# Kernel optimization log

Measured on AMD Instinct MI355X. Metric: run time of the kernel, lower is better.

The kernel has to match this reference:

```python
import jax, jax.numpy as jnp
import numpy as np

B, S, D, H, F = 4, 2048, 256, 8, 2  # batch, seq, input_size, heads, mlp factor
EPS = 1e-5


def _ln(x, g, b):
    m = jnp.mean(x, axis=-1, keepdims=True)
    v = jnp.var(x, axis=-1, keepdims=True)
    return (x - m) / jnp.sqrt(v + EPS) * g + b


def setup_inputs() -> dict:
    key = jax.random.key(0)
    ks = jax.random.split(key, 12)
    s = 1.0 / np.sqrt(D)
    return {
        "X":  jax.random.normal(ks[0], (B, S, D), jnp.float32),
        # Wide attention: each of H heads has full [D,D] Q/K/V projections (no bias)
        "Wq": jax.random.uniform(ks[1], (H, D, D), jnp.float32, -s, s),
        "Wk": jax.random.uniform(ks[2], (H, D, D), jnp.float32, -s, s),
        "Wv": jax.random.uniform(ks[3], (H, D, D), jnp.float32, -s, s),
        "Wz": jax.random.uniform(ks[4], (H * D, D), jnp.float32, -1.0 / np.sqrt(H * D), 1.0 / np.sqrt(H * D)),
        "bz": jnp.zeros((D,), jnp.float32),
        "W1": jax.random.uniform(ks[5], (D, F * D), jnp.float32, -s, s),
        "b1": jnp.zeros((F * D,), jnp.float32),
        "W2": jax.random.uniform(ks[6], (F * D, D), jnp.float32, -1.0 / np.sqrt(F * D), 1.0 / np.sqrt(F * D)),
        "b2": jnp.zeros((D,), jnp.float32),
        "g1": jnp.ones((D,), jnp.float32),
        "be1": jnp.zeros((D,), jnp.float32),
        "g2": jnp.ones((D,), jnp.float32),
        "be2": jnp.zeros((D,), jnp.float32),
    }


def reference(X, Wq, Wk, Wv, Wz, bz, W1, b1, W2, b2, g1, be1, g2, be2):
    scale = D ** (-0.25)  # applied to both q and k as in the source
    q = jnp.einsum('bsd,hde->hbse', X, Wq) * scale   # [H,B,S,D]
    k = jnp.einsum('btd,hde->hbte', X, Wk) * scale
    v = jnp.einsum('btd,hde->hbte', X, Wv)
    attn = jax.nn.softmax(jnp.einsum('hbse,hbte->hbst', q, k), axis=-1)  # [H,B,S,S]
    zh = jnp.einsum('hbst,hbte->hbse', attn, v)       # [H,B,S,D]
    # concat heads along feature dim (head order matters for Wz)
    zcat = jnp.transpose(zh, (1, 2, 0, 3)).reshape(B, S, H * D)
    z = zcat @ Wz + bz
    z = _ln(z + X, g1, be1)                            # dropout p=0 -> identity
    z_ff = jnp.maximum(z @ W1 + b1, 0.0) @ W2 + b2
    z = _ln(z_ff + z, g2, be2)
    attn_mean = jnp.mean(attn, axis=0)                 # [B,S,S]
    return z, attn_mean
```

## Files before the change

kernel.cpp:

```cpp
#include <hip/hip_runtime.h>
#include <cstdint>
#include <cstddef>

#define B_  4
#define S_  2048
#define D_  256
#define H_  8
#define FD_ 512
#define N_  (B_*S_)
#define HD_ (H_*D_)
#define EPS 1e-5f

typedef __attribute__((ext_vector_type(8))) short bf16x8;
typedef __attribute__((ext_vector_type(8))) unsigned short u16x8;
typedef __attribute__((ext_vector_type(4))) float f32x4;

__device__ __forceinline__ unsigned short f2bf(float f) {
  union { float f; unsigned u; } x; x.f = f;
  unsigned u = x.u;
  return (unsigned short)((u + 0x7FFFu + ((u >> 16) & 1u)) >> 16);
}
__device__ __forceinline__ float bf2f(unsigned short h) {
  union { unsigned u; float f; } x; x.u = ((unsigned)h) << 16; return x.f;
}

__device__ __forceinline__ void glds16(const void* gptr, void* ldsptr) {
  __builtin_amdgcn_global_load_lds(
      (__attribute__((address_space(1))) void*)gptr,
      (__attribute__((address_space(3))) void*)ldsptr,
      16, 0, 0);
}

__device__ __forceinline__ int sw32(int row, int u) {
  return (row*32 + ((u & 24) | ((u & 7) ^ (row & 7)))) * 8;
}
__device__ __forceinline__ int sw16(int row, int u) {
  return (row*16 + ((u & 8) | ((u & 7) ^ (row & 7)))) * 8;
}

__global__ __launch_bounds__(256) void cast_x_kernel(
    const float* __restrict__ X, unsigned short* __restrict__ Xb)
{
  const size_t i8 = ((size_t)blockIdx.x * 256 + threadIdx.x) * 8;
  float4 a = *(const float4*)&X[i8];
  float4 b = *(const float4*)&X[i8 + 4];
  u16x8 o;
  o[0]=f2bf(a.x); o[1]=f2bf(a.y); o[2]=f2bf(a.z); o[3]=f2bf(a.w);
  o[4]=f2bf(b.x); o[5]=f2bf(b.y); o[6]=f2bf(b.z); o[7]=f2bf(b.w);
  *(u16x8*)&Xb[i8] = o;
}

__global__ __launch_bounds__(256) void prep_w_kernel(
    const float* __restrict__ Wq, const float* __restrict__ Wk,
    const float* __restrict__ Wv, unsigned short* __restrict__ Wt)
{
  __shared__ float tile[64][65];
  const int tid = threadIdx.x;
  const int d0 = blockIdx.x * 64, e0 = blockIdx.y * 64;
  const int w = blockIdx.z;
  const float* src;
  float scale;
  if (w < 8)       { src = Wq + (size_t)w*D_*D_;      scale = 0.25f; }
  else if (w < 16) { src = Wk + (size_t)(w-8)*D_*D_;  scale = 0.25f; }
  else             { src = Wv + (size_t)(w-16)*D_*D_; scale = 1.0f;  }
  {
    int r = tid >> 2, c16 = (tid & 3) * 16;
    const float* s = src + (size_t)(d0 + r)*D_ + e0 + c16;
    #pragma unroll
    for (int u = 0; u < 4; ++u) *(float4*)&tile[r][c16 + u*4] = *(const float4*)(s + u*4);
  }
  __syncthreads();
  {
    int er = tid >> 2, dc = (tid & 3) * 16;
    u16x8 o0, o1;
    #pragma unroll
    for (int j = 0; j < 8; ++j) {
      o0[j] = f2bf(tile[dc + j][er] * scale);
      o1[j] = f2bf(tile[dc + 8 + j][er] * scale);
    }
    unsigned short* dst = Wt + ((size_t)w*D_ + e0 + er)*D_ + d0 + dc;
    *(u16x8*)(dst)     = o0;
    *(u16x8*)(dst + 8) = o1;
  }
}

__global__ __launch_bounds__(256) void tcast_kernel(
    const float* __restrict__ src, unsigned short* __restrict__ dst,
    int R, int C)
{
  __shared__ float tile[64][65];
  const int tid = threadIdx.x;
  const int r0 = blockIdx.x * 64, c0 = blockIdx.y * 64;
  {
    int r = tid >> 2, c16 = (tid & 3) * 16;
    const float* s = src + (size_t)(r0 + r)*C + c0 + c16;
    #pragma unroll
    for (int u = 0; u < 4; ++u) *(float4*)&tile[r][c16 + u*4] = *(const float4*)(s + u*4);
  }
  __syncthreads();
  {
    int cr = tid >> 2, rc = (tid & 3) * 16;
    u16x8 o0, o1;
    #pragma unroll
    for (int j = 0; j < 8; ++j) {
      o0[j] = f2bf(tile[rc + j][cr]);
      o1[j] = f2bf(tile[rc + 8 + j][cr]);
    }
    unsigned short* d = dst + (size_t)(c0 + cr)*R + r0 + rc;
    *(u16x8*)(d)     = o0;
    *(u16x8*)(d + 8) = o1;
  }
}

__global__ __launch_bounds__(256) void qkv_kernel(
    const unsigned short* __restrict__ Xb, const unsigned short* __restrict__ Wt,
    unsigned short* __restrict__ q, unsigned short* __restrict__ k,
    unsigned short* __restrict__ v)
{
  __shared__ unsigned short Xt[64*32*8];
  __shared__ unsigned short Wtile[64*32*8];
  const int tid = threadIdx.x;
  const int w4 = tid >> 6, lane = tid & 63;
  const int c = lane & 15, qd = lane >> 4;
  const int n0 = blockIdx.x * 64;
  const int e0 = blockIdx.y * 64;
  const int w  = blockIdx.z;

  unsigned short* obase;
  if (w < 8)       obase = q + (size_t)w*N_*D_;
  else if (w < 16) obase = k + (size_t)(w-8)*N_*D_;
  else             obase = v + (size_t)(w-16)*N_*D_;

  {
    const char* xg = (const char*)Xb + (size_t)n0*512;
    const char* wg = (const char*)Wt + ((size_t)w*D_ + e0)*512;
    #pragma unroll
    for (int i = 0; i < 8; ++i) {
      int g = w4*8 + i;
      int r = 2*g + (lane >> 5);
      int su = lane & 31;
      int u = (su & 24) | ((su & 7) ^ (r & 7));
      glds16(xg + (size_t)r*512 + u*16, &Xt[g*512]);
      glds16(wg + (size_t)r*512 + u*16, &Wtile[g*512]);
    }
  }
  __syncthreads();

  f32x4 sc[4];
  #pragma unroll
  for (int nc = 0; nc < 4; ++nc) sc[nc] = (f32x4){0.f,0.f,0.f,0.f};
  #pragma unroll
  for (int ks = 0; ks < 8; ++ks) {
    bf16x8 xa = *(const bf16x8*)&Xt[sw32(16*w4 + c, ks*4 + qd)];
    #pragma unroll
    for (int nc = 0; nc < 4; ++nc) {
      bf16x8 bf = *(const bf16x8*)&Wtile[sw32(nc*16 + c, ks*4 + qd)];
      sc[nc] = __builtin_amdgcn_mfma_f32_16x16x32_bf16(xa, bf, sc[nc], 0, 0, 0);
    }
  }
  #pragma unroll
  for (int nc = 0; nc < 4; ++nc)
    #pragma unroll
    for (int r = 0; r < 4; ++r)
      obase[(size_t)(n0 + 16*w4 + qd*4 + r)*D_ + e0 + nc*16 + c] = f2bf(sc[nc][r]);
}

__global__ __launch_bounds__(256) void vtrans_kernel(
    const unsigned short* __restrict__ vb, unsigned short* __restrict__ vT)
{
  __shared__ unsigned short tile[64][72];
  const int tid = threadIdx.x;
  const int t0 = blockIdx.x * 64, e0 = blockIdx.y * 64;
  const int h = blockIdx.z >> 2, b = blockIdx.z & 3;
  const size_t in_base = (size_t)h*N_*D_ + (size_t)b*S_*D_;
  {
    int r = tid >> 2, c16 = (tid & 3) * 16;
    const unsigned short* src = vb + in_base + (size_t)(t0 + r)*D_ + e0 + c16;
    *(u16x8*)&tile[r][c16]     = *(const u16x8*)(src);
    *(u16x8*)&tile[r][c16 + 8] = *(const u16x8*)(src + 8);
  }
  __syncthreads();
  {
    int er = tid >> 2, tt = (tid & 3) * 16;
    u16x8 o0, o1;
    #pragma unroll
    for (int j = 0; j < 8; ++j) { o0[j] = tile[tt+j][er]; o1[j] = tile[tt+8+j][er]; }
    unsigned short* dst = vT + ((size_t)(h*4 + b)*D_ + e0 + er)*S_ + t0 + tt;
    *(u16x8*)(dst)     = o0;
    *(u16x8*)(dst + 8) = o1;
  }
}

__global__ __launch_bounds__(256, 2) void attn_ol_kernel(
    const unsigned short* __restrict__ qb, const unsigned short* __restrict__ kb,
    const unsigned short* __restrict__ vT, unsigned short* __restrict__ zcatb,
    float* __restrict__ Lws)
{
  __shared__ unsigned short Kt[2][32*32*8];
  __shared__ unsigned short Vt[2][16*544];
  __shared__ unsigned short ps[4][32][40];
  const int tid = threadIdx.x;
  const int w = tid >> 6, lane = tid & 63;
  const int c = lane & 15, qd = lane >> 4;
  const int s0 = blockIdx.x * 128;
  const int b = blockIdx.y, h = blockIdx.z;

  const size_t qkbase = (size_t)h*N_*D_ + (size_t)b*S_*D_;

  bf16x8 qa[2][8];
  #pragma unroll
  for (int mi = 0; mi < 2; ++mi) {
    const unsigned short* qrow = qb + qkbase + (size_t)(s0 + 32*w + 16*mi + c)*D_ + qd*8;
    #pragma unroll
    for (int ks = 0; ks < 8; ++ks) qa[mi][ks] = *(const bf16x8*)(qrow + ks*32);
  }

  f32x4 o[2][16];
  #pragma unroll
  for (int mi = 0; mi < 2; ++mi)
    #pragma unroll
    for (int i = 0; i < 16; ++i) o[mi][i] = (f32x4){0.f,0.f,0.f,0.f};
  float Lp[2][4] = {};

  const char* kB = (const char*)(kb + qkbase);
  const char* vB = (const char*)(vT + (size_t)(h*4 + b)*D_*S_);

  #define STAGE_OL(kt_, bi_)                                                   \
    {                                                                          \
      _Pragma("unroll")                                                        \
      for (int i = 0; i < 4; ++i) {                                            \
        int g = w*4 + i;                                                       \
        int r = 2*g + (lane >> 5);                                             \
        int su = lane & 31;                                                    \
        int u = (su & 24) | ((su & 7) ^ (r & 7));                              \
        glds16(kB + ((size_t)(kt_)*32 + r)*512 + u*16, &Kt[bi_][g*512]);       \
      }                                                                        \
      _Pragma("unroll")                                                        \
      for (int i = 0; i < 4; ++i) {                                            \
        int g = w*4 + i;                                                       \
        int e = g*16 + (lane >> 2);                                            \
        int qv = (lane & 3) ^ ((lane >> 3) & 3);                               \
        glds16(vB + (size_t)e*4096 + (size_t)(kt_)*64 + qv*16, &Vt[bi_][g*544]);\
      }                                                                        \
    }

  STAGE_OL(0, 0);

  for (int kt = 0; kt < 64; ++kt) {
    const int bi = kt & 1;
    __syncthreads();
    if (kt + 1 < 64) STAGE_OL(kt + 1, bi ^ 1);

    f32x4 sc[2][2];
    #pragma unroll
    for (int mi = 0; mi < 2; ++mi)
      #pragma unroll
      for (int nc = 0; nc < 2; ++nc) sc[mi][nc] = (f32x4){0.f,0.f,0.f,0.f};
    #pragma unroll
    for (int ks = 0; ks < 8; ++ks) {
      bf16x8 kf0 = *(const bf16x8*)&Kt[bi][sw32(c,      ks*4 + qd)];
      bf16x8 kf1 = *(const bf16x8*)&Kt[bi][sw32(16 + c, ks*4 + qd)];
      #pragma unroll
      for (int mi = 0; mi < 2; ++mi) {
        sc[mi][0] = __builtin_amdgcn_mfma_f32_16x16x32_bf16(qa[mi][ks], kf0, sc[mi][0], 0, 0, 0);
        sc[mi][1] = __builtin_amdgcn_mfma_f32_16x16x32_bf16(qa[mi][ks], kf1, sc[mi][1], 0, 0, 0);
      }
    }
    #pragma unroll
    for (int mi = 0; mi < 2; ++mi)
      #pragma unroll
      for (int nc = 0; nc < 2; ++nc)
        #pragma unroll
        for (int r = 0; r < 4; ++r) {
          float p = __expf(sc[mi][nc][r]);
          Lp[mi][r] += p;
          ps[w][mi*16 + qd*4 + r][nc*16 + c] = f2bf(p);
        }
    bf16x8 pa0 = *(const bf16x8*)&ps[w][c][qd*8];
    bf16x8 pa1 = *(const bf16x8*)&ps[w][16 + c][qd*8];
    #pragma unroll
    for (int ec = 0; ec < 16; ++ec) {
      bf16x8 vf = *(const bf16x8*)&Vt[bi][ec*544 + c*32 + (qd ^ ((c >> 1) & 3))*8];
      o[0][ec] = __builtin_amdgcn_mfma_f32_16x16x32_bf16(pa0, vf, o[0][ec], 0, 0, 0);
      o[1][ec] = __builtin_amdgcn_mfma_f32_16x16x32_bf16(pa1, vf, o[1][ec], 0, 0, 0);
    }
  }

  #pragma unroll
  for (int mi = 0; mi < 2; ++mi) {
    float il[4];
    #pragma unroll
    for (int r = 0; r < 4; ++r) {
      float L = Lp[mi][r];
      L += __shfl_xor(L, 1); L += __shfl_xor(L, 2);
      L += __shfl_xor(L, 4); L += __shfl_xor(L, 8);
      Lp[mi][r] = L;
      il[r] = 1.0f / L;
    }
    if (c == 0) {
      #pragma unroll
      for (int r = 0; r < 4; ++r)
        Lws[(size_t)h*N_ + b*S_ + s0 + 32*w + 16*mi + qd*4 + r] = Lp[mi][r];
    }
    #pragma unroll
    for (int ec = 0; ec < 16; ++ec)
      #pragma unroll
      for (int r = 0; r < 4; ++r)
        zcatb[(size_t)(b*S_ + s0 + 32*w + 16*mi + qd*4 + r)*HD_ + h*D_ + ec*16 + c] =
            f2bf(o[mi][ec][r] * il[r]);
  }
  #undef STAGE_OL
}

__global__ __launch_bounds__(256, 2) void attn_mean_kernel(
    const unsigned short* __restrict__ qb, const unsigned short* __restrict__ kb,
    const float* __restrict__ Lws, float* __restrict__ out_attn)
{
  __shared__ unsigned short Kt[2][64*32*8];
  const int tid = threadIdx.x;
  const int w = tid >> 6, lane = tid & 63;
  const int c = lane & 15, qd = lane >> 4;
  const int s0 = blockIdx.x * 128;
  const int t0 = blockIdx.y * 64;
  const int b = blockIdx.z;

  float am[2][4][4] = {};

  #define STAGE_AM(h_, bi_)                                                    \
    {                                                                          \
      const char* kB = (const char*)(kb + (size_t)(h_)*N_*D_ + (size_t)b*S_*D_);\
      _Pragma("unroll")                                                        \
      for (int i = 0; i < 8; ++i) {                                            \
        int g = w*8 + i;                                                       \
        int r = 2*g + (lane >> 5);                                             \
        int su = lane & 31;                                                    \
        int u = (su & 24) | ((su & 7) ^ (r & 7));                              \
        glds16(kB + ((size_t)t0 + r)*512 + u*16, &Kt[bi_][g*512]);             \
      }                                                                        \
    }

  STAGE_AM(0, 0);

  for (int h = 0; h < 8; ++h) {
    const int bi = h & 1;
    __syncthreads();
    if (h + 1 < 8) STAGE_AM(h + 1, bi ^ 1);

    const size_t base = (size_t)h*N_*D_ + (size_t)b*S_*D_;
    bf16x8 qa[2][8];
    #pragma unroll
    for (int mi = 0; mi < 2; ++mi) {
      const unsigned short* qrow = qb + base + (size_t)(s0 + 32*w + 16*mi + c)*D_ + qd*8;
      #pragma unroll
      for (int ks = 0; ks < 8; ++ks) qa[mi][ks] = *(const bf16x8*)(qrow + ks*32);
    }
    f32x4 sc[2][4];
    #pragma unroll
    for (int mi = 0; mi < 2; ++mi)
      #pragma unroll
      for (int nc = 0; nc < 4; ++nc) sc[mi][nc] = (f32x4){0.f,0.f,0.f,0.f};
    #pragma unroll
    for (int ks = 0; ks < 8; ++ks) {
      #pragma unroll
      for (int nc = 0; nc < 4; ++nc) {
        bf16x8 kf = *(const bf16x8*)&Kt[bi][sw32(nc*16 + c, ks*4 + qd)];
        sc[0][nc] = __builtin_amdgcn_mfma_f32_16x16x32_bf16(qa[0][ks], kf, sc[0][nc], 0, 0, 0);
        sc[1][nc] = __builtin_amdgcn_mfma_f32_16x16x32_bf16(qa[1][ks], kf, sc[1][nc], 0, 0, 0);
      }
    }
    #pragma unroll
    for (int mi = 0; mi < 2; ++mi) {
      float il8[4];
      #pragma unroll
      for (int r = 0; r < 4; ++r)
        il8[r] = 0.125f / Lws[(size_t)h*N_ + b*S_ + s0 + 32*w + 16*mi + qd*4 + r];
      #pragma unroll
      for (int nc = 0; nc < 4; ++nc)
        #pragma unroll
        for (int r = 0; r < 4; ++r)
          am[mi][nc][r] += __expf(sc[mi][nc][r]) * il8[r];
    }
  }
  #pragma unroll
  for (int mi = 0; mi < 2; ++mi)
    #pragma unroll
    for (int nc = 0; nc < 4; ++nc)
      #pragma unroll
      for (int r = 0; r < 4; ++r)
        out_attn[(size_t)(b*S_ + s0 + 32*w + 16*mi + qd*4 + r)*S_ + t0 + nc*16 + c] =
            am[mi][nc][r];
  #undef STAGE_AM
}

__global__ __launch_bounds__(256) void wz_ln1_kernel(
    const unsigned short* __restrict__ zcatb, const unsigned short* __restrict__ Wzt,
    const float* __restrict__ bz, const float* __restrict__ X,
    const float* __restrict__ g1, const float* __restrict__ be1,
    unsigned short* __restrict__ z1b)
{
  __shared__ unsigned short At[32*16*8];
  __shared__ unsigned short Wt2[256*16*8];
  __shared__ float redS[2][32], redQ[2][32];
  const int tid = threadIdx.x;
  const int w4 = tid >> 6, lane = tid & 63;
  const int c = lane & 15, qd = lane >> 4;
  const int n0 = blockIdx.x * 32;
  const int msub = w4 & 1, ehalf = w4 >> 1;

  f32x4 acc[8];
  #pragma unroll
  for (int nc = 0; nc < 8; ++nc) acc[nc] = (f32x4){0.f,0.f,0.f,0.f};

  for (int kc = 0; kc < 16; ++kc) {
    {
      const char* ab = (const char*)zcatb + (size_t)n0*4096 + (size_t)kc*256;
      #pragma unroll
      for (int i = 0; i < 2; ++i) {
        int g = w4*2 + i;
        int r = g*4 + (lane >> 4);
        int su = lane & 15;
        int u = (su & 8) | ((su & 7) ^ (r & 7));
        glds16(ab + (size_t)r*4096 + u*16, &At[g*512]);
      }
      const char* wb = (const char*)Wzt + (size_t)kc*256;
      #pragma unroll
      for (int i = 0; i < 16; ++i) {
        int g = w4*16 + i;
        int e = g*4 + (lane >> 4);
        int su = lane & 15;
        int u = (su & 8) | ((su & 7) ^ (e & 7));
        glds16(wb + (size_t)e*4096 + u*16, &Wt2[g*512]);
      }
    }
    __syncthreads();
    #pragma unroll
    for (int ks = 0; ks < 4; ++ks) {
      bf16x8 a = *(const bf16x8*)&At[sw16(msub*16 + c, ks*4 + qd)];
      #pragma unroll
      for (int nc = 0; nc < 8; ++nc) {
        bf16x8 bv = *(const bf16x8*)&Wt2[sw16(ehalf*128 + nc*16 + c, ks*4 + qd)];
        acc[nc] = __builtin_amdgcn_mfma_f32_16x16x32_bf16(a, bv, acc[nc], 0, 0, 0);
      }
    }
    __syncthreads();
  }

  float vals[8][4];
  float sum_[4] = {0.f,0.f,0.f,0.f}, sq_[4] = {0.f,0.f,0.f,0.f};
  #pragma unroll
  for (int nc = 0; nc < 8; ++nc) {
    int e = ehalf*128 + nc*16 + c;
    #pragma unroll
    for (int r = 0; r < 4; ++r) {
      int n = n0 + msub*16 + qd*4 + r;
      float v = acc[nc][r] + bz[e] + X[(size_t)n*D_ + e];
      vals[nc][r] = v;
      sum_[r] += v; sq_[r] += v*v;
    }
  }
  #pragma unroll
  for (int off = 1; off < 16; off <<= 1) {
    #pragma unroll
    for (int r = 0; r < 4; ++r) {
      sum_[r] += __shfl_xor(sum_[r], off);
      sq_[r]  += __shfl_xor(sq_[r],  off);
    }
  }
  if (c == 0) {
    #pragma unroll
    for (int r = 0; r < 4; ++r) {
      redS[ehalf][msub*16 + qd*4 + r] = sum_[r];
      redQ[ehalf][msub*16 + qd*4 + r] = sq_[r];
    }
  }
  __syncthreads();
  #pragma unroll
  for (int r = 0; r < 4; ++r) {
    int lr = msub*16 + qd*4 + r;
    float Sv = redS[0][lr] + redS[1][lr];
    float Qv = redQ[0][lr] + redQ[1][lr];
    float mean = Sv * (1.0f/D_);
    float var  = Qv * (1.0f/D_) - mean*mean;
    float rstd = rsqrtf(var + EPS);
    int n = n0 + lr;
    #pragma unroll
    for (int nc = 0; nc < 8; ++nc) {
      int e = ehalf*128 + nc*16 + c;
      z1b[(size_t)n*D_ + e] = f2bf((vals[nc][r] - mean)*rstd*g1[e] + be1[e]);
    }
  }
}

__global__ __launch_bounds__(256) void mlp1_kernel(
    const unsigned short* __restrict__ z1b, const unsigned short* __restrict__ W1t,
    const float* __restrict__ b1, unsigned short* __restrict__ hbuf)
{
  __shared__ unsigned short At[64*32*8];
  __shared__ unsigned short Bt[64*32*8];
  const int tid = threadIdx.x;
  const int w4 = tid >> 6, lane = tid & 63;
  const int c = lane & 15, qd = lane >> 4;
  const int n0 = blockIdx.x * 64;
  const int f0 = blockIdx.y * 64;

  {
    const char* ag = (const char*)z1b + (size_t)n0*512;
    const char* bg = (const char*)W1t + (size_t)f0*512;
    #pragma unroll
    for (int i = 0; i < 8; ++i) {
      int g = w4*8 + i;
      int r = 2*g + (lane >> 5);
      int su = lane & 31;
      int u = (su & 24) | ((su & 7) ^ (r & 7));
      glds16(ag + (size_t)r*512 + u*16, &At[g*512]);
      glds16(bg + (size_t)r*512 + u*16, &Bt[g*512]);
    }
  }
  __syncthreads();

  f32x4 sc[4];
  #pragma unroll
  for (int nc = 0; nc < 4; ++nc) sc[nc] = (f32x4){0.f,0.f,0.f,0.f};
  #pragma unroll
  for (int ks = 0; ks < 8; ++ks) {
    bf16x8 xa = *(const bf16x8*)&At[sw32(16*w4 + c, ks*4 + qd)];
    #pragma unroll
    for (int nc = 0; nc < 4; ++nc) {
      bf16x8 bf = *(const bf16x8*)&Bt[sw32(nc*16 + c, ks*4 + qd)];
      sc[nc] = __builtin_amdgcn_mfma_f32_16x16x32_bf16(xa, bf, sc[nc], 0, 0, 0);
    }
  }
  #pragma unroll
  for (int nc = 0; nc < 4; ++nc) {
    int f = f0 + nc*16 + c;
    float bias = b1[f];
    #pragma unroll
    for (int r = 0; r < 4; ++r)
      hbuf[(size_t)(n0 + 16*w4 + qd*4 + r)*FD_ + f] = f2bf(fmaxf(sc[nc][r] + bias, 0.f));
  }
}

__global__ __launch_bounds__(256) void mlp2_kernel(
    const unsigned short* __restrict__ hbuf, const unsigned short* __restrict__ W2t,
    const float* __restrict__ b2, const unsigned short* __restrict__ z1b,
    const float* __restrict__ g2, const float* __restrict__ be2,
    float* __restrict__ out)
{
  __shared__ unsigned short At[32*16*8];
  __shared__ unsigned short Wt2[256*16*8];
  __shared__ float redS[2][32], redQ[2][32];
  const int tid = threadIdx.x;
  const int w4 = tid >> 6, lane = tid & 63;
  const int c = lane & 15, qd = lane >> 4;
  const int n0 = blockIdx.x * 32;
  const int msub = w4 & 1, ehalf = w4 >> 1;

  f32x4 acc[8];
  #pragma unroll
  for (int nc = 0; nc < 8; ++nc) acc[nc] = (f32x4){0.f,0.f,0.f,0.f};

  for (int kc = 0; kc < 4; ++kc) {
    {
      const char* ab = (const char*)hbuf + (size_t)n0*1024 + (size_t)kc*256;
      #pragma unroll
      for (int i = 0; i < 2; ++i) {
        int g = w4*2 + i;
        int r = g*4 + (lane >> 4);
        int su = lane & 15;
        int u = (su & 8) | ((su & 7) ^ (r & 7));
        glds16(ab + (size_t)r*1024 + u*16, &At[g*512]);
      }
      const char* wb = (const char*)W2t + (size_t)kc*256;
      #pragma unroll
      for (int i = 0; i < 16; ++i) {
        int g = w4*16 + i;
        int e = g*4 + (lane >> 4);
        int su = lane & 15;
        int u = (su & 8) | ((su & 7) ^ (e & 7));
        glds16(wb + (size_t)e*1024 + u*16, &Wt2[g*512]);
      }
    }
    __syncthreads();
    #pragma unroll
    for (int ks = 0; ks < 4; ++ks) {
      bf16x8 a = *(const bf16x8*)&At[sw16(msub*16 + c, ks*4 + qd)];
      #pragma unroll
      for (int nc = 0; nc < 8; ++nc) {
        bf16x8 bv = *(const bf16x8*)&Wt2[sw16(ehalf*128 + nc*16 + c, ks*4 + qd)];
        acc[nc] = __builtin_amdgcn_mfma_f32_16x16x32_bf16(a, bv, acc[nc], 0, 0, 0);
      }
    }
    __syncthreads();
  }

  float vals[8][4];
  float sum_[4] = {0.f,0.f,0.f,0.f}, sq_[4] = {0.f,0.f,0.f,0.f};
  #pragma unroll
  for (int nc = 0; nc < 8; ++nc) {
    int e = ehalf*128 + nc*16 + c;
    #pragma unroll
    for (int r = 0; r < 4; ++r) {
      int n = n0 + msub*16 + qd*4 + r;
      float v = acc[nc][r] + b2[e] + bf2f(z1b[(size_t)n*D_ + e]);
      vals[nc][r] = v;
      sum_[r] += v; sq_[r] += v*v;
    }
  }
  #pragma unroll
  for (int off = 1; off < 16; off <<= 1) {
    #pragma unroll
    for (int r = 0; r < 4; ++r) {
      sum_[r] += __shfl_xor(sum_[r], off);
      sq_[r]  += __shfl_xor(sq_[r],  off);
    }
  }
  if (c == 0) {
    #pragma unroll
    for (int r = 0; r < 4; ++r) {
      redS[ehalf][msub*16 + qd*4 + r] = sum_[r];
      redQ[ehalf][msub*16 + qd*4 + r] = sq_[r];
    }
  }
  __syncthreads();
  #pragma unroll
  for (int r = 0; r < 4; ++r) {
    int lr = msub*16 + qd*4 + r;
    float Sv = redS[0][lr] + redS[1][lr];
    float Qv = redQ[0][lr] + redQ[1][lr];
    float mean = Sv * (1.0f/D_);
    float var  = Qv * (1.0f/D_) - mean*mean;
    float rstd = rsqrtf(var + EPS);
    int n = n0 + lr;
    #pragma unroll
    for (int nc = 0; nc < 8; ++nc) {
      int e = ehalf*128 + nc*16 + c;
      out[(size_t)n*D_ + e] = (vals[nc][r] - mean)*rstd*g2[e] + be2[e];
    }
  }
}

extern "C" void kernel_launch(void* const* d_in, const int* in_sizes, int n_in,
                              void* d_out, int out_size, void* d_ws, size_t ws_size,
                              hipStream_t stream)
{
  (void)in_sizes; (void)n_in; (void)out_size; (void)ws_size;
  const float* X   = (const float*)d_in[0];
  const float* Wq  = (const float*)d_in[1];
  const float* Wk  = (const float*)d_in[2];
  const float* Wv  = (const float*)d_in[3];
  const float* Wz  = (const float*)d_in[4];
  const float* bz  = (const float*)d_in[5];
  const float* W1  = (const float*)d_in[6];
  const float* b1  = (const float*)d_in[7];
  const float* W2  = (const float*)d_in[8];
  const float* b2  = (const float*)d_in[9];
  const float* g1  = (const float*)d_in[10];
  const float* be1 = (const float*)d_in[11];
  const float* g2  = (const float*)d_in[12];
  const float* be2 = (const float*)d_in[13];

  char* p = (char*)d_ws;
  unsigned short* Xbb  = (unsigned short*)p; p += (size_t)N_*D_*2;
  unsigned short* Wtb  = (unsigned short*)p; p += (size_t)24*D_*D_*2;
  unsigned short* Wztb = (unsigned short*)p; p += (size_t)D_*HD_*2;
  unsigned short* W1tb = (unsigned short*)p; p += (size_t)FD_*D_*2;
  unsigned short* W2tb = (unsigned short*)p; p += (size_t)D_*FD_*2;
  unsigned short* qbuf = (unsigned short*)p; p += (size_t)H_*N_*D_*2;
  unsigned short* kbuf = (unsigned short*)p; p += (size_t)H_*N_*D_*2;
  unsigned short* vbuf = (unsigned short*)p; p += (size_t)H_*N_*D_*2;
  unsigned short* vTb  = (unsigned short*)p; p += (size_t)H_*N_*D_*2;
  float* Lws   = (float*)p; p += (size_t)H_*N_*4;
  unsigned short* zcatb = (unsigned short*)p; p += (size_t)N_*HD_*2;
  unsigned short* z1b   = (unsigned short*)p; p += (size_t)N_*D_*2;
  unsigned short* hbuf  = (unsigned short*)p;

  float* out_z    = (float*)d_out;
  float* out_attn = out_z + (size_t)N_*D_;

  cast_x_kernel<<<N_*D_/(256*8), 256, 0, stream>>>(X, Xbb);

  dim3 gW(4, 4, 24);
  prep_w_kernel<<<gW, 256, 0, stream>>>(Wq, Wk, Wv, Wtb);

  { dim3 g(HD_/64, D_/64);  tcast_kernel<<<g, 256, 0, stream>>>(Wz, Wztb, HD_, D_); }
  { dim3 g(D_/64, FD_/64);  tcast_kernel<<<g, 256, 0, stream>>>(W1, W1tb, D_, FD_); }
  { dim3 g(FD_/64, D_/64);  tcast_kernel<<<g, 256, 0, stream>>>(W2, W2tb, FD_, D_); }

  dim3 gA(N_/64, D_/64, 24);
  qkv_kernel<<<gA, 256, 0, stream>>>(Xbb, Wtb, qbuf, kbuf, vbuf);

  dim3 gT(S_/64, D_/64, H_*B_);
  vtrans_kernel<<<gT, 256, 0, stream>>>(vbuf, vTb);

  dim3 gB1(S_/128, B_, H_);
  attn_ol_kernel<<<gB1, 256, 0, stream>>>(qbuf, kbuf, vTb, zcatb, Lws);

  dim3 gB2(S_/128, S_/64, B_);
  attn_mean_kernel<<<gB2, 256, 0, stream>>>(qbuf, kbuf, Lws, out_attn);

  wz_ln1_kernel<<<N_/32, 256, 0, stream>>>(zcatb, Wztb, bz, X, g1, be1, z1b);

  dim3 gM1(N_/64, FD_/64);
  mlp1_kernel<<<gM1, 256, 0, stream>>>(z1b, W1tb, b1, hbuf);

  mlp2_kernel<<<N_/32, 256, 0, stream>>>(hbuf, W2tb, b2, z1b, g2, be2, out_z);
}
```

Before: 554.8 us.

## Keep softmax probabilities in registers by transposing QK^T MFMA and permuting K rows

The score MFMA now takes K as the A operand and Q as B, so each lane holds scores for a single query row. K rows are loaded into shared memory under a permutation chosen so that the lane's accumulator values line up with the A-operand layout of the P·V MFMA. The probabilities are packed to bf16 with v_cvt_pk_bf16_f32 and fed straight into P·V, which removes the per-wave shared-memory round trip through the ps buffer. The row-sum reduction shrinks to two cross-lane shuffles, and a shfl redistributes the inverse sums back to the output layout. The risk is that the permutation is subtle, and a wrong mapping would silently corrupt results.

```diff
diff --git a/kernel.cpp b/kernel.cpp
--- a/kernel.cpp
+++ b/kernel.cpp
@@ -198,7 +198,6 @@
 {
   __shared__ unsigned short Kt[2][32*32*8];
   __shared__ unsigned short Vt[2][16*544];
-  __shared__ unsigned short ps[4][32][40];
   const int tid = threadIdx.x;
   const int w = tid >> 6, lane = tid & 63;
   const int c = lane & 15, qd = lane >> 4;
@@ -220,7 +219,7 @@
   for (int mi = 0; mi < 2; ++mi)
     #pragma unroll
     for (int i = 0; i < 16; ++i) o[mi][i] = (f32x4){0.f,0.f,0.f,0.f};
-  float Lp[2][4] = {};
+  float Lp[2] = {0.f, 0.f};
 
   const char* kB = (const char*)(kb + qkbase);
   const char* vB = (const char*)(vT + (size_t)(h*4 + b)*D_*S_);
@@ -231,9 +230,10 @@
       for (int i = 0; i < 4; ++i) {                                            \
         int g = w*4 + i;                                                       \
         int r = 2*g + (lane >> 5);                                             \
+        int Lg = ((r >> 2) & 3)*8 + (r >> 4)*4 + (r & 3);                      \
         int su = lane & 31;                                                    \
         int u = (su & 24) | ((su & 7) ^ (r & 7));                              \
-        glds16(kB + ((size_t)(kt_)*32 + r)*512 + u*16, &Kt[bi_][g*512]);       \
+        glds16(kB + ((size_t)(kt_)*32 + Lg)*512 + u*16, &Kt[bi_][g*512]);      \
       }                                                                        \
       _Pragma("unroll")                                                        \
       for (int i = 0; i < 4; ++i) {                                            \
@@ -262,46 +262,48 @@
       bf16x8 kf1 = *(const bf16x8*)&Kt[bi][sw32(16 + c, ks*4 + qd)];
       #pragma unroll
       for (int mi = 0; mi < 2; ++mi) {
-        sc[mi][0] = __builtin_amdgcn_mfma_f32_16x16x32_bf16(qa[mi][ks], kf0, sc[mi][0], 0, 0, 0);
-        sc[mi][1] = __builtin_amdgcn_mfma_f32_16x16x32_bf16(qa[mi][ks], kf1, sc[mi][1], 0, 0, 0);
+        sc[mi][0] = __builtin_amdgcn_mfma_f32_16x16x32_bf16(kf0, qa[mi][ks], sc[mi][0], 0, 0, 0);
+        sc[mi][1] = __builtin_amdgcn_mfma_f32_16x16x32_bf16(kf1, qa[mi][ks], sc[mi][1], 0, 0, 0);
       }
     }
-    #pragma unroll
-    for (int mi = 0; mi < 2; ++mi)
+    bf16x8 pa[2];
+    #pragma unroll
+    for (int mi = 0; mi < 2; ++mi) {
+      float ex[2][4];
       #pragma unroll
       for (int nc = 0; nc < 2; ++nc)
         #pragma unroll
         for (int r = 0; r < 4; ++r) {
           float p = __expf(sc[mi][nc][r]);
-          Lp[mi][r] += p;
-          ps[w][mi*16 + qd*4 + r][nc*16 + c] = f2bf(p);
+          ex[nc][r] = p;
+          Lp[mi] += p;
         }
-    bf16x8 pa0 = *(const bf16x8*)&ps[w][c][qd*8];
-    bf16x8 pa1 = *(const bf16x8*)&ps[w][16 + c][qd*8];
+      union { unsigned u[4]; bf16x8 v; } cv;
+      asm("v_cvt_pk_bf16_f32 %0, %1, %2" : "=v"(cv.u[0]) : "v"(ex[0][0]), "v"(ex[0][1]));
+      asm("v_cvt_pk_bf16_f32 %0, %1, %2" : "=v"(cv.u[1]) : "v"(ex[0][2]), "v"(ex[0][3]));
+      asm("v_cvt_pk_bf16_f32 %0, %1, %2" : "=v"(cv.u[2]) : "v"(ex[1][0]), "v"(ex[1][1]));
+      asm("v_cvt_pk_bf16_f32 %0, %1, %2" : "=v"(cv.u[3]) : "v"(ex[1][2]), "v"(ex[1][3]));
+      pa[mi] = cv.v;
+    }
     #pragma unroll
     for (int ec = 0; ec < 16; ++ec) {
       bf16x8 vf = *(const bf16x8*)&Vt[bi][ec*544 + c*32 + (qd ^ ((c >> 1) & 3))*8];
-      o[0][ec] = __builtin_amdgcn_mfma_f32_16x16x32_bf16(pa0, vf, o[0][ec], 0, 0, 0);
-      o[1][ec] = __builtin_amdgcn_mfma_f32_16x16x32_bf16(pa1, vf, o[1][ec], 0, 0, 0);
+      o[0][ec] = __builtin_amdgcn_mfma_f32_16x16x32_bf16(pa[0], vf, o[0][ec], 0, 0, 0);
+      o[1][ec] = __builtin_amdgcn_mfma_f32_16x16x32_bf16(pa[1], vf, o[1][ec], 0, 0, 0);
     }
   }
 
   #pragma unroll
   for (int mi = 0; mi < 2; ++mi) {
+    float L = Lp[mi];
+    L += __shfl_xor(L, 16);
+    L += __shfl_xor(L, 32);
+    if (qd == 0)
+      Lws[(size_t)h*N_ + b*S_ + s0 + 32*w + 16*mi + c] = L;
     float il[4];
     #pragma unroll
-    for (int r = 0; r < 4; ++r) {
-      float L = Lp[mi][r];
-      L += __shfl_xor(L, 1); L += __shfl_xor(L, 2);
-      L += __shfl_xor(L, 4); L += __shfl_xor(L, 8);
-      Lp[mi][r] = L;
-      il[r] = 1.0f / L;
-    }
-    if (c == 0) {
-      #pragma unroll
-      for (int r = 0; r < 4; ++r)
-        Lws[(size_t)h*N_ + b*S_ + s0 + 32*w + 16*mi + qd*4 + r] = Lp[mi][r];
-    }
+    for (int r = 0; r < 4; ++r)
+      il[r] = 1.0f / __shfl(L, (lane & 48) | (qd*4 + r));
     #pragma unroll
     for (int ec = 0; ec < 16; ++ec)
       #pragma unroll
```

Result: faster. 536.0 us (-3.4%).
